# Kernel optimization log

Measured on AMD Instinct MI355X. Metric: run time of the kernel, lower is better.

The kernel has to match this reference:

```python
import jax, jax.numpy as jnp
import numpy as np

N = 50000; E = 800000
HID = 64; HEADS = 8; DH = HID // HEADS; L = 6
VOC = 512; NSIGN = 3; SIGN_DIM = 8; EDGE_DIM = 16; EPS = 1e-5


def setup_inputs() -> dict:
    key = jax.random.key(0)
    ks = jax.random.split(key, 24)
    s = 0.05
    rn = lambda k, sh: jax.random.normal(k, sh, jnp.float32) * s
    return dict(
        x_nodes=jax.random.randint(ks[0], (N, 4), 0, VOC),
        edge_index=jax.random.randint(ks[1], (2, E), 0, N),
        edge_label=jax.random.randint(ks[2], (E,), 0, VOC),
        edge_sign=jax.random.randint(ks[3], (E,), 0, NSIGN),
        emb_strand=rn(ks[4], (VOC, HID)),
        emb_pos=rn(ks[5], (4, HID)),
        emb_sign=rn(ks[6], (NSIGN, SIGN_DIM)),
        We=rn(ks[7], (HID + SIGN_DIM, EDGE_DIM)), be=jnp.zeros((EDGE_DIM,), jnp.float32),
        Wq=rn(ks[8], (L, HID, HID)), bq=jnp.zeros((L, HID), jnp.float32),
        Wk=rn(ks[9], (L, HID, HID)), bk=jnp.zeros((L, HID), jnp.float32),
        Wv=rn(ks[10], (L, HID, HID)), bv=jnp.zeros((L, HID), jnp.float32),
        Wedge=rn(ks[11], (L, EDGE_DIM, HID)),
        Wskip=rn(ks[12], (L, HID, HID)), bskip=jnp.zeros((L, HID), jnp.float32),
        ln_g=jnp.ones((L - 1, HID), jnp.float32), ln_b=jnp.zeros((L - 1, HID), jnp.float32),
        Wp=rn(ks[13], (HID, 2)), bp=jnp.zeros((2,), jnp.float32),
        Wv1=rn(ks[14], (HID, HID)), bv1=jnp.zeros((HID,), jnp.float32),
        Wv2=rn(ks[15], (HID, 1)), bv2=jnp.zeros((1,), jnp.float32),
    )


def _layernorm(x, g, b):
    mu = x.mean(-1, keepdims=True)
    var = jnp.mean((x - mu) ** 2, -1, keepdims=True)
    return g * (x - mu) / jnp.sqrt(var + EPS) + b


def reference(x_nodes, edge_index, edge_label, edge_sign,
              emb_strand, emb_pos, emb_sign, We, be,
              Wq, bq, Wk, bk, Wv, bv, Wedge, Wskip, bskip,
              ln_g, ln_b, Wp, bp, Wv1, bv1, Wv2, bv2):
    src, dst = edge_index[0], edge_index[1]
    # node features: per-crossing strand embeddings + positional embeddings, summed over 4 slots
    x = (emb_strand[x_nodes] + emb_pos[None, :, :]).sum(axis=1)  # [N, HID]
    # edge features: [strand_emb | sign_emb] -> Linear(24 -> 16)
    ef = jnp.concatenate([emb_strand[edge_label], emb_sign[edge_sign]], -1) @ We + be  # [E, 16]
    scale = 1.0 / jnp.sqrt(jnp.float32(DH))
    for l in range(L):
        q = (x @ Wq[l] + bq[l]).reshape(N, HEADS, DH)
        k = (x @ Wk[l] + bk[l]).reshape(N, HEADS, DH)
        v = (x @ Wv[l] + bv[l]).reshape(N, HEADS, DH)
        e = (ef @ Wedge[l]).reshape(E, HEADS, DH)  # lin_edge has no bias in PyG
        kj = k[src] + e  # [E, H, DH]
        alpha = (q[dst] * kj).sum(-1) * scale  # [E, H]
        m = jax.ops.segment_max(alpha, dst, num_segments=N)  # per-target softmax
        a = jnp.exp(alpha - m[dst])
        ssum = jax.ops.segment_sum(a, dst, num_segments=N)
        a = a / (ssum[dst] + 1e-16)
        msg = (v[src] + e) * a[:, :, None]
        out = jax.ops.segment_sum(msg, dst, num_segments=N).reshape(N, HID)
        out = out + x @ Wskip[l] + bskip[l]  # root_weight skip connection
        if l < L - 1:
            x = jax.nn.relu(_layernorm(out, ln_g[l], ln_b[l]))
        else:
            x = out
    policy = (x @ Wp + bp).reshape(1, -1)  # single-graph path: [1, 2N]
    g = x.mean(0, keepdims=True)  # [1, HID]
    val = jnp.tanh(jax.nn.relu(g @ Wv1 + bv1) @ Wv2 + bv2)  # [1, 1]
    return (policy, val)
```

## Files before the change

### kernel.cpp

```cpp
#include <hip/hip_runtime.h>
#include <math.h>

typedef _Float16 f16;
typedef _Float16 f16x8 __attribute__((ext_vector_type(8)));
typedef float f32x4 __attribute__((ext_vector_type(4)));

#define N_NODES 50000
#define N_EDGES 800000
#define HID 64
#define HEADS 8
#define DH 8
#define LAYERS 6
#define EDGE_DIM 16
#define SIGN_DIM 8
#define NSIGN 3
#define VOC 512
#define NCOMB (VOC * NSIGN)
#define EPS 1e-5f

#define NBUCK 196
#define BUCK_CAP 5120
#define BIN_EPB 4096
#define BIN_EPT 16
#define BIN_NBLK ((N_EDGES + BIN_EPB - 1) / BIN_EPB)

__device__ __forceinline__ float dot8(f16x8 a, f16x8 b, float c) {
#if __has_builtin(__builtin_amdgcn_fdot2)
    c = __builtin_amdgcn_fdot2(__builtin_shufflevector(a, a, 0, 1),
                               __builtin_shufflevector(b, b, 0, 1), c, false);
    c = __builtin_amdgcn_fdot2(__builtin_shufflevector(a, a, 2, 3),
                               __builtin_shufflevector(b, b, 2, 3), c, false);
    c = __builtin_amdgcn_fdot2(__builtin_shufflevector(a, a, 4, 5),
                               __builtin_shufflevector(b, b, 4, 5), c, false);
    c = __builtin_amdgcn_fdot2(__builtin_shufflevector(a, a, 6, 7),
                               __builtin_shufflevector(b, b, 6, 7), c, false);
#else
#pragma unroll
    for (int i = 0; i < 8; ++i) c += (float)a[i] * (float)b[i];
#endif
    return c;
}

__global__ __launch_bounds__(256) void k_node_feat(
    const int* __restrict__ xn, const float* __restrict__ emb_s,
    const float* __restrict__ emb_p, f16* __restrict__ x16) {
    int idx = blockIdx.x * 256 + threadIdx.x;
    if (idx >= N_NODES * HID) return;
    int n = idx >> 6, d = idx & 63;
    float acc = 0.f;
#pragma unroll
    for (int s = 0; s < 4; ++s) {
        int id = xn[n * 4 + s];
        acc += emb_s[id * HID + d] + emb_p[s * HID + d];
    }
    x16[idx] = (f16)acc;
}

__global__ __launch_bounds__(256) void k_tabTE(
    const float* __restrict__ emb_s, const float* __restrict__ emb_sg,
    const float* __restrict__ We, const float* __restrict__ be,
    const float* __restrict__ Wedge, f16* __restrict__ TE) {
    __shared__ float T[16][16];
    int t = threadIdx.x;
    int comb0 = blockIdx.x * 16;
    int cl = t >> 4, c = t & 15;
    int comb = comb0 + cl;
    int lb = comb / NSIGN, sg = comb % NSIGN;
    float acc = be[c];
    const float* er = emb_s + lb * HID;
#pragma unroll
    for (int j = 0; j < HID; ++j) acc += er[j] * We[j * EDGE_DIM + c];
    const float* sr = emb_sg + sg * SIGN_DIM;
#pragma unroll
    for (int j = 0; j < SIGN_DIM; ++j) acc += sr[j] * We[(HID + j) * EDGE_DIM + c];
    T[cl][c] = acc;
    __syncthreads();
    for (int l = 0; l < LAYERS; ++l) {
        const float* w = Wedge + l * EDGE_DIM * HID;
#pragma unroll
        for (int rep = 0; rep < 4; ++rep) {
            int idx = rep * 256 + t;
            int cml = idx >> 6, d = idx & 63;
            float a = 0.f;
#pragma unroll
            for (int j = 0; j < EDGE_DIM; ++j) a += T[cml][j] * w[j * HID + d];
            TE[((size_t)l * NCOMB + comb0 + cml) * HID + d] = (f16)a;
        }
    }
}

__global__ __launch_bounds__(256) void k_wprep(
    const float* __restrict__ Wq, const float* __restrict__ bq,
    const float* __restrict__ Wk, const float* __restrict__ bk,
    const float* __restrict__ Wv, const float* __restrict__ bv,
    const float* __restrict__ Ws, const float* __restrict__ bs,
    f16* __restrict__ wcatT, float* __restrict__ bcat) {
    int idx = blockIdx.x * 256 + threadIdx.x;
    if (idx >= LAYERS * 256 * HID) return;
    int l = idx >> 14;
    int r = idx & 16383;
    int c = r >> 6, kk = r & 63;
    int m = c >> 6, cc = c & 63;
    const float* W = (m == 0) ? Wq : (m == 1) ? Wk : (m == 2) ? Wv : Ws;
    wcatT[idx] = (f16)W[l * 4096 + kk * 64 + cc];
    if (kk == 0) {
        const float* B = (m == 0) ? bq : (m == 1) ? bk : (m == 2) ? bv : bs;
        bcat[l * 256 + c] = B[l * 64 + cc];
    }
}

__global__ __launch_bounds__(256) void k_bin(
    const int* __restrict__ src, const int* __restrict__ dst,
    const int* __restrict__ label, const int* __restrict__ sign,
    int* __restrict__ bcur, int2* __restrict__ buf) {
    __shared__ int hist[NBUCK];
    __shared__ int base[NBUCK];
    int t = threadIdx.x;
    for (int i = t; i < NBUCK; i += 256) hist[i] = 0;
    __syncthreads();
    int e0 = blockIdx.x * BIN_EPB;
    int pk[BIN_EPT], dl[BIN_EPT], bl[BIN_EPT], loc[BIN_EPT];
#pragma unroll
    for (int i = 0; i < BIN_EPT; ++i) {
        int e = e0 + i * 256 + t;
        bool vld = e < N_EDGES;
        int d = vld ? dst[e] : 0;
        bl[i] = d >> 8;
        dl[i] = d & 255;
        pk[i] = vld ? ((src[e] << 11) | (label[e] * NSIGN + sign[e])) : 0;
        loc[i] = vld ? atomicAdd(&hist[bl[i]], 1) : -1;
    }
    __syncthreads();
    if (t < NBUCK) {
        int h = hist[t];
        int gb = h ? atomicAdd(&bcur[t], h) : 0;
        base[t] = t * BUCK_CAP + gb;
    }
    __syncthreads();
#pragma unroll
    for (int i = 0; i < BIN_EPT; ++i)
        if (loc[i] >= 0) buf[base[bl[i]] + loc[i]] = make_int2(pk[i], dl[i]);
}

__global__ __launch_bounds__(256) void k_bscan(
    const int* __restrict__ bcur, int* __restrict__ bbase,
    int* __restrict__ rowptr, float* __restrict__ gsum) {
    __shared__ int ws[4];
    int t = threadIdx.x;
    int lane = t & 63, w = t >> 6;
    int v = (t < NBUCK) ? bcur[t] : 0;
    int incl = v;
#pragma unroll
    for (int o = 1; o < 64; o <<= 1) {
        int u = __shfl_up(incl, o);
        if (lane >= o) incl += u;
    }
    if (lane == 63) ws[w] = incl;
    __syncthreads();
    int woff = 0;
    for (int j = 0; j < w; ++j) woff += ws[j];
    if (t < NBUCK) bbase[t] = woff + incl - v;
    if (t == 0) rowptr[N_NODES] = N_EDGES;
    if (t < 64) gsum[t] = 0.f;
}

__global__ __launch_bounds__(256) void k_place(
    const int* __restrict__ bcur, const int* __restrict__ bbase,
    const int2* __restrict__ buf, int* __restrict__ rowptr,
    int* __restrict__ scomb) {
    __shared__ int hist[256];
    __shared__ int curs[256];
    __shared__ int ws[4];
    int t = threadIdx.x, b = blockIdx.x;
    hist[t] = 0;
    __syncthreads();
    int cnt = bcur[b];
    const int2* bb = buf + (size_t)b * BUCK_CAP;
    for (int i = t; i < cnt; i += 256) atomicAdd(&hist[bb[i].y], 1);
    __syncthreads();
    int v = hist[t];
    int lane = t & 63, w = t >> 6;
    int incl = v;
#pragma unroll
    for (int o = 1; o < 64; o <<= 1) {
        int u = __shfl_up(incl, o);
        if (lane >= o) incl += u;
    }
    if (lane == 63) ws[w] = incl;
    __syncthreads();
    int woff = 0;
    for (int j = 0; j < w; ++j) woff += ws[j];
    int start = bbase[b] + woff + incl - v;
    int n = (b << 8) + t;
    if (n < N_NODES) rowptr[n] = start;
    curs[t] = start;
    __syncthreads();
    for (int i = t; i < cnt; i += 256) {
        int2 r = bb[i];
        int pos = atomicAdd(&curs[r.y], 1);
        scomb[pos] = r.x;
    }
}

__global__ __launch_bounds__(256) void k_proj(
    const f16* __restrict__ x16, const f16* __restrict__ wcatT_l,
    const float* __restrict__ bcat_l,
    f16* __restrict__ q, f16* __restrict__ kv, f16* __restrict__ sk) {
    int t = threadIdx.x;
    int w = t >> 6, l = t & 63;
    int n0 = blockIdx.x * 16;
    int rowA = n0 + (l & 15);
    int kb = l >> 4;
    const f16* xr = x16 + (rowA << 6) + (kb << 3);
    f16x8 a0 = *(const f16x8*)(xr);
    f16x8 a1 = *(const f16x8*)(xr + 32);
    int c0 = w << 6;
    int rbase = n0 + ((l >> 4) << 2);
#pragma unroll
    for (int tt = 0; tt < 4; ++tt) {
        int cl = c0 + tt * 16 + (l & 15);
        const f16* wr = wcatT_l + (cl << 6) + (kb << 3);
        f16x8 b0 = *(const f16x8*)(wr);
        f16x8 b1 = *(const f16x8*)(wr + 32);
        f32x4 z = {0.f, 0.f, 0.f, 0.f};
        z = __builtin_amdgcn_mfma_f32_16x16x32_f16(a0, b0, z, 0, 0, 0);
        z = __builtin_amdgcn_mfma_f32_16x16x32_f16(a1, b1, z, 0, 0, 0);
        float bb = bcat_l[cl];
        int cc = cl & 63;
#pragma unroll
        for (int r = 0; r < 4; ++r) {
            int n = rbase + r;
            f16 val = (f16)(z[r] + bb);
            if (w == 0) q[(n << 6) + cc] = val;
            else if (w == 1) kv[(size_t)n * 128 + cc] = val;
            else if (w == 2) kv[(size_t)n * 128 + 64 + cc] = val;
            else sk[(n << 6) + cc] = val;
        }
    }
}

__global__ __launch_bounds__(256) void k_agg(
    const f16* __restrict__ q, const f16* __restrict__ kv,
    const f16* __restrict__ sk, const f16* __restrict__ te,
    const int* __restrict__ scomb, const int* __restrict__ rowptr,
    const float* __restrict__ ln_g, const float* __restrict__ ln_b,
    f16* __restrict__ xout, int do_ln,
    const float* __restrict__ Wp, const float* __restrict__ bp,
    float* __restrict__ pol) {
    int t = threadIdx.x;
    int wid = t >> 6, lane = t & 63;
    int n = blockIdx.x * 4 + wid;
    if (n >= N_NODES) return;
    int e = lane >> 3;
    int h = lane & 7;
    f16x8 qf = *(const f16x8*)(q + (n << 6) + (h << 3));
    int rs = rowptr[n], re = rowptr[n + 1];
    const float scale = 0.35355339059327373f;
    float lsum = 0.f;
    float acc0 = 0.f, acc1 = 0.f, acc2 = 0.f, acc3 = 0.f;
    float acc4 = 0.f, acc5 = 0.f, acc6 = 0.f, acc7 = 0.f;
    for (int j0 = rs; j0 < re; j0 += 16) {
        int ja = j0 + e, jb = j0 + 8 + e;
        bool va = ja < re, vb = jb < re;
        int pa = scomb[va ? ja : rs];
        int pb = scomb[vb ? jb : rs];
        const f16* kpa = kv + ((size_t)(pa >> 11) << 7) + (h << 3);
        const f16* kpb = kv + ((size_t)(pb >> 11) << 7) + (h << 3);
        f16x8 ka = *(const f16x8*)(kpa);
        f16x8 vaf = *(const f16x8*)(kpa + 64);
        f16x8 ta = *(const f16x8*)(te + ((pa & 2047) << 6) + (h << 3));
        f16x8 kb2 = *(const f16x8*)(kpb);
        f16x8 vbf = *(const f16x8*)(kpb + 64);
        f16x8 tb = *(const f16x8*)(te + ((pb & 2047) << 6) + (h << 3));
        float ala = dot8(qf, ka + ta, 0.f) * scale;
        float alb = dot8(qf, kb2 + tb, 0.f) * scale;
        float wa = va ? __expf(ala) : 0.f;
        float wb = vb ? __expf(alb) : 0.f;
        lsum += wa + wb;
        f16x8 vta = vaf + ta;
        f16x8 vtb = vbf + tb;
        acc0 += wa * (float)vta[0] + wb * (float)vtb[0];
        acc1 += wa * (float)vta[1] + wb * (float)vtb[1];
        acc2 += wa * (float)vta[2] + wb * (float)vtb[2];
        acc3 += wa * (float)vta[3] + wb * (float)vtb[3];
        acc4 += wa * (float)vta[4] + wb * (float)vtb[4];
        acc5 += wa * (float)vta[5] + wb * (float)vtb[5];
        acc6 += wa * (float)vta[6] + wb * (float)vtb[6];
        acc7 += wa * (float)vta[7] + wb * (float)vtb[7];
    }
#pragma unroll
    for (int o = 8; o < 64; o <<= 1) {
        lsum += __shfl_xor(lsum, o);
        acc0 += __shfl_xor(acc0, o);
        acc1 += __shfl_xor(acc1, o);
        acc2 += __shfl_xor(acc2, o);
        acc3 += __shfl_xor(acc3, o);
        acc4 += __shfl_xor(acc4, o);
        acc5 += __shfl_xor(acc5, o);
        acc6 += __shfl_xor(acc6, o);
        acc7 += __shfl_xor(acc7, o);
    }
    float av = acc0;
    av = (e == 1) ? acc1 : av;
    av = (e == 2) ? acc2 : av;
    av = (e == 3) ? acc3 : av;
    av = (e == 4) ? acc4 : av;
    av = (e == 5) ? acc5 : av;
    av = (e == 6) ? acc6 : av;
    av = (e == 7) ? acc7 : av;
    int d = (h << 3) + e;
    float outv = av / (lsum + 1e-16f) + (float)sk[(n << 6) + d];
    if (do_ln) {
        float ssum = outv;
#pragma unroll
        for (int o = 1; o < 64; o <<= 1) ssum += __shfl_xor(ssum, o);
        float mu = ssum * (1.f / 64.f);
        float dv = outv - mu;
        float vs = dv * dv;
#pragma unroll
        for (int o = 1; o < 64; o <<= 1) vs += __shfl_xor(vs, o);
        float var = vs * (1.f / 64.f);
        float yv = ln_g[d] * dv / sqrtf(var + EPS) + ln_b[d];
        outv = fmaxf(yv, 0.f);
        xout[(n << 6) + d] = (f16)outv;
    } else {
        xout[(n << 6) + d] = (f16)outv;
        float p0 = outv * Wp[d * 2 + 0];
        float p1 = outv * Wp[d * 2 + 1];
#pragma unroll
        for (int o = 1; o < 64; o <<= 1) {
            p0 += __shfl_xor(p0, o);
            p1 += __shfl_xor(p1, o);
        }
        if (lane == 0) {
            pol[n * 2 + 0] = p0 + bp[0];
            pol[n * 2 + 1] = p1 + bp[1];
        }
    }
}

__global__ __launch_bounds__(256) void k_colsum(const f16* __restrict__ x16, float* __restrict__ gsum) {
    __shared__ float sh[256];
    int t = threadIdx.x;
    int col = t & 63;
    float acc = 0.f;
    for (int n = blockIdx.x * 4 + (t >> 6); n < N_NODES; n += gridDim.x * 4)
        acc += (float)x16[(n << 6) + col];
    sh[t] = acc;
    __syncthreads();
    if (t < 64) {
        float s = sh[t] + sh[t + 64] + sh[t + 128] + sh[t + 192];
        atomicAdd(&gsum[t], s);
    }
}

__global__ __launch_bounds__(64) void k_value(
    const float* __restrict__ gsum, const float* __restrict__ Wv1,
    const float* __restrict__ bv1, const float* __restrict__ Wv2,
    const float* __restrict__ bv2, float* __restrict__ out) {
    int lane = threadIdx.x;
    float h = bv1[lane];
    for (int i = 0; i < HID; ++i) h += (gsum[i] * (1.f / N_NODES)) * Wv1[i * HID + lane];
    h = fmaxf(h, 0.f);
    float p = h * Wv2[lane];
#pragma unroll
    for (int o = 1; o < 64; o <<= 1) p += __shfl_xor(p, o);
    if (lane == 0) out[0] = tanhf(p + bv2[0]);
}

extern "C" void kernel_launch(void* const* d_in, const int* in_sizes, int n_in,
                              void* d_out, int out_size, void* d_ws, size_t ws_size,
                              hipStream_t stream) {
    const int* x_nodes = (const int*)d_in[0];
    const int* edge_index = (const int*)d_in[1];
    const int* edge_label = (const int*)d_in[2];
    const int* edge_sign = (const int*)d_in[3];
    const float* emb_strand = (const float*)d_in[4];
    const float* emb_pos = (const float*)d_in[5];
    const float* emb_sign = (const float*)d_in[6];
    const float* We = (const float*)d_in[7];
    const float* be = (const float*)d_in[8];
    const float* Wq = (const float*)d_in[9];
    const float* bq = (const float*)d_in[10];
    const float* Wk = (const float*)d_in[11];
    const float* bk = (const float*)d_in[12];
    const float* Wv = (const float*)d_in[13];
    const float* bv = (const float*)d_in[14];
    const float* Wedge = (const float*)d_in[15];
    const float* Wskip = (const float*)d_in[16];
    const float* bskip = (const float*)d_in[17];
    const float* ln_g = (const float*)d_in[18];
    const float* ln_b = (const float*)d_in[19];
    const float* Wp = (const float*)d_in[20];
    const float* bp = (const float*)d_in[21];
    const float* Wv1 = (const float*)d_in[22];
    const float* bv1 = (const float*)d_in[23];
    const float* Wv2 = (const float*)d_in[24];
    const float* bv2 = (const float*)d_in[25];
    float* out = (float*)d_out;

    const int* src = edge_index;
    const int* dst = edge_index + N_EDGES;

    char* ws = (char*)d_ws;
    size_t off = 0;
    auto alloc = [&](size_t bytes) -> void* {
        void* p = ws + off;
        off += (bytes + 255) & ~(size_t)255;
        return p;
    };
    f16* x16 = (f16*)alloc((size_t)N_NODES * HID * 2);
    f16* q = (f16*)alloc((size_t)N_NODES * HID * 2);
    f16* kv = (f16*)alloc((size_t)N_NODES * 128 * 2);
    f16* sk = (f16*)alloc((size_t)N_NODES * HID * 2);
    int* scomb = (int*)alloc((size_t)N_EDGES * 4);
    int2* binbuf = (int2*)alloc((size_t)NBUCK * BUCK_CAP * 8);
    int* rowptr = (int*)alloc((size_t)(N_NODES + 1) * 4);
    int* bcur = (int*)alloc((size_t)NBUCK * 4);
    int* bbase = (int*)alloc((size_t)NBUCK * 4);
    f16* TE = (f16*)alloc((size_t)LAYERS * NCOMB * HID * 2);
    f16* wcatT = (f16*)alloc((size_t)LAYERS * 256 * HID * 2);
    float* bcat = (float*)alloc((size_t)LAYERS * 256 * 4);
    float* gsum = (float*)alloc(64 * 4);

    hipMemsetAsync(bcur, 0, (size_t)NBUCK * 4, stream);

    k_node_feat<<<(N_NODES * HID + 255) / 256, 256, 0, stream>>>(x_nodes, emb_strand, emb_pos, x16);
    k_tabTE<<<NCOMB / 16, 256, 0, stream>>>(emb_strand, emb_sign, We, be, Wedge, TE);
    k_wprep<<<(LAYERS * 256 * HID + 255) / 256, 256, 0, stream>>>(
        Wq, bq, Wk, bk, Wv, bv, Wskip, bskip, wcatT, bcat);
    k_bin<<<BIN_NBLK, 256, 0, stream>>>(src, dst, edge_label, edge_sign, bcur, binbuf);
    k_bscan<<<1, 256, 0, stream>>>(bcur, bbase, rowptr, gsum);
    k_place<<<NBUCK, 256, 0, stream>>>(bcur, bbase, binbuf, rowptr, scomb);

    for (int l = 0; l < LAYERS; ++l) {
        k_proj<<<N_NODES / 16, 256, 0, stream>>>(
            x16, wcatT + (size_t)l * 256 * HID, bcat + (size_t)l * 256, q, kv, sk);
        int do_ln = (l < LAYERS - 1) ? 1 : 0;
        const float* lg = do_ln ? (ln_g + (size_t)l * HID) : ln_g;
        const float* lb = do_ln ? (ln_b + (size_t)l * HID) : ln_b;
        k_agg<<<(N_NODES + 3) / 4, 256, 0, stream>>>(
            q, kv, sk, TE + (size_t)l * NCOMB * HID, scomb, rowptr,
            lg, lb, x16, do_ln, Wp, bp, out);
    }

    k_colsum<<<128, 256, 0, stream>>>(x16, gsum);
    k_value<<<1, 64, 0, stream>>>(gsum, Wv1, bv1, Wv2, bv2, out + 2 * N_NODES);
}
```

Measured before the change: 423.7 us.

## Fuse next-layer projection into aggregation kernel and merge setup kernels

The aggregation kernel for layers 0-4 now applies layernorm+relu, stages the 4 node rows in shared memory, and runs the next layer's QKV/skip projection with MFMA directly. This removes the separate projection launches and the x16 round trip through global memory. Q/KV/skip buffers are ping-ponged across layers. The three setup kernels and the memset are folded into one block-dispatched kernel. The fused projection pads each 4-row tile to 16 MFMA rows, wasting three quarters of the matrix work, and it adds a block-wide barrier after the irregular per-node aggregation.

```diff
diff --git a/kernel.cpp b/kernel.cpp
--- a/kernel.cpp
+++ b/kernel.cpp
@@ -24,6 +24,11 @@
 #define BIN_EPT 16
 #define BIN_NBLK ((N_EDGES + BIN_EPB - 1) / BIN_EPB)
 
+#define NF_BLK 12500
+#define WP_BLK 384
+#define TE_BLK (LAYERS * (NCOMB / 16))
+#define SETUP_BLK (NF_BLK + WP_BLK + TE_BLK + 1)
+
 __device__ __forceinline__ float dot8(f16x8 a, f16x8 b, float c) {
 #if __has_builtin(__builtin_amdgcn_fdot2)
     c = __builtin_amdgcn_fdot2(__builtin_shufflevector(a, a, 0, 1),
@@ -41,41 +46,63 @@
     return c;
 }
 
-__global__ __launch_bounds__(256) void k_node_feat(
+__global__ __launch_bounds__(256) void k_setup(
     const int* __restrict__ xn, const float* __restrict__ emb_s,
-    const float* __restrict__ emb_p, f16* __restrict__ x16) {
-    int idx = blockIdx.x * 256 + threadIdx.x;
-    if (idx >= N_NODES * HID) return;
-    int n = idx >> 6, d = idx & 63;
-    float acc = 0.f;
-#pragma unroll
-    for (int s = 0; s < 4; ++s) {
-        int id = xn[n * 4 + s];
-        acc += emb_s[id * HID + d] + emb_p[s * HID + d];
-    }
-    x16[idx] = (f16)acc;
-}
-
-__global__ __launch_bounds__(256) void k_tabTE(
-    const float* __restrict__ emb_s, const float* __restrict__ emb_sg,
-    const float* __restrict__ We, const float* __restrict__ be,
-    const float* __restrict__ Wedge, f16* __restrict__ TE) {
-    __shared__ float T[16][16];
-    int t = threadIdx.x;
-    int comb0 = blockIdx.x * 16;
-    int cl = t >> 4, c = t & 15;
-    int comb = comb0 + cl;
-    int lb = comb / NSIGN, sg = comb % NSIGN;
-    float acc = be[c];
-    const float* er = emb_s + lb * HID;
-#pragma unroll
-    for (int j = 0; j < HID; ++j) acc += er[j] * We[j * EDGE_DIM + c];
-    const float* sr = emb_sg + sg * SIGN_DIM;
-#pragma unroll
-    for (int j = 0; j < SIGN_DIM; ++j) acc += sr[j] * We[(HID + j) * EDGE_DIM + c];
-    T[cl][c] = acc;
-    __syncthreads();
-    for (int l = 0; l < LAYERS; ++l) {
+    const float* __restrict__ emb_p, f16* __restrict__ x16,
+    const float* __restrict__ Wq, const float* __restrict__ bq,
+    const float* __restrict__ Wk, const float* __restrict__ bk,
+    const float* __restrict__ Wv, const float* __restrict__ bv,
+    const float* __restrict__ Ws, const float* __restrict__ bs,
+    f16* __restrict__ wcatT, float* __restrict__ bcat,
+    const float* __restrict__ emb_sg, const float* __restrict__ We,
+    const float* __restrict__ be, const float* __restrict__ Wedge,
+    f16* __restrict__ TE, int* __restrict__ bcur) {
+    int b = blockIdx.x;
+    int t = threadIdx.x;
+    if (b < NF_BLK) {
+        int idx = b * 256 + t;
+        int n = idx >> 6, d = idx & 63;
+        float acc = 0.f;
+#pragma unroll
+        for (int s = 0; s < 4; ++s) {
+            int id = xn[n * 4 + s];
+            acc += emb_s[id * HID + d] + emb_p[s * HID + d];
+        }
+        x16[idx] = (f16)acc;
+        return;
+    }
+    b -= NF_BLK;
+    if (b < WP_BLK) {
+        int idx = b * 256 + t;
+        int l = idx >> 14;
+        int r = idx & 16383;
+        int c = r >> 6, kk = r & 63;
+        int m = c >> 6, cc = c & 63;
+        const float* W = (m == 0) ? Wq : (m == 1) ? Wk : (m == 2) ? Wv : Ws;
+        wcatT[idx] = (f16)W[l * 4096 + kk * 64 + cc];
+        if (kk == 0) {
+            const float* B = (m == 0) ? bq : (m == 1) ? bk : (m == 2) ? bv : bs;
+            bcat[l * 256 + c] = B[l * 64 + cc];
+        }
+        return;
+    }
+    b -= WP_BLK;
+    if (b < TE_BLK) {
+        __shared__ float T[16][16];
+        int l = b / (NCOMB / 16);
+        int comb0 = (b % (NCOMB / 16)) * 16;
+        int cl = t >> 4, c = t & 15;
+        int comb = comb0 + cl;
+        int lb = comb / NSIGN, sg = comb % NSIGN;
+        float acc = be[c];
+        const float* er = emb_s + lb * HID;
+#pragma unroll
+        for (int j = 0; j < HID; ++j) acc += er[j] * We[j * EDGE_DIM + c];
+        const float* sr = emb_sg + sg * SIGN_DIM;
+#pragma unroll
+        for (int j = 0; j < SIGN_DIM; ++j) acc += sr[j] * We[(HID + j) * EDGE_DIM + c];
+        T[cl][c] = acc;
+        __syncthreads();
         const float* w = Wedge + l * EDGE_DIM * HID;
 #pragma unroll
         for (int rep = 0; rep < 4; ++rep) {
@@ -86,27 +113,9 @@
             for (int j = 0; j < EDGE_DIM; ++j) a += T[cml][j] * w[j * HID + d];
             TE[((size_t)l * NCOMB + comb0 + cml) * HID + d] = (f16)a;
         }
-    }
-}
-
-__global__ __launch_bounds__(256) void k_wprep(
-    const float* __restrict__ Wq, const float* __restrict__ bq,
-    const float* __restrict__ Wk, const float* __restrict__ bk,
-    const float* __restrict__ Wv, const float* __restrict__ bv,
-    const float* __restrict__ Ws, const float* __restrict__ bs,
-    f16* __restrict__ wcatT, float* __restrict__ bcat) {
-    int idx = blockIdx.x * 256 + threadIdx.x;
-    if (idx >= LAYERS * 256 * HID) return;
-    int l = idx >> 14;
-    int r = idx & 16383;
-    int c = r >> 6, kk = r & 63;
-    int m = c >> 6, cc = c & 63;
-    const float* W = (m == 0) ? Wq : (m == 1) ? Wk : (m == 2) ? Wv : Ws;
-    wcatT[idx] = (f16)W[l * 4096 + kk * 64 + cc];
-    if (kk == 0) {
-        const float* B = (m == 0) ? bq : (m == 1) ? bk : (m == 2) ? bv : bs;
-        bcat[l * 256 + c] = B[l * 64 + cc];
-    }
+        return;
+    }
+    if (t < NBUCK) bcur[t] = 0;
 }
 
 __global__ __launch_bounds__(256) void k_bin(
@@ -239,20 +248,23 @@
     }
 }
 
-__global__ __launch_bounds__(256) void k_agg(
+__global__ __launch_bounds__(256) void k_aggP(
     const f16* __restrict__ q, const f16* __restrict__ kv,
     const f16* __restrict__ sk, const f16* __restrict__ te,
     const int* __restrict__ scomb, const int* __restrict__ rowptr,
     const float* __restrict__ ln_g, const float* __restrict__ ln_b,
-    f16* __restrict__ xout, int do_ln,
-    const float* __restrict__ Wp, const float* __restrict__ bp,
-    float* __restrict__ pol) {
+    const f16* __restrict__ wcat_nx, const float* __restrict__ bcat_nx,
+    f16* __restrict__ q_o, f16* __restrict__ kv_o, f16* __restrict__ sk_o) {
+    __shared__ __align__(16) f16 xs[16][64];
     int t = threadIdx.x;
     int wid = t >> 6, lane = t & 63;
-    int n = blockIdx.x * 4 + wid;
-    if (n >= N_NODES) return;
+    int n0 = blockIdx.x * 4;
+    int n = n0 + wid;
+    for (int i = t; i < 768; i += 256) ((f16*)xs)[256 + i] = (f16)0.f;
     int e = lane >> 3;
     int h = lane & 7;
+    int d = (h << 3) + e;
+    float skv = (float)sk[(n << 6) + d];
     f16x8 qf = *(const f16x8*)(q + (n << 6) + (h << 3));
     int rs = rowptr[n], re = rowptr[n + 1];
     const float scale = 0.35355339059327373f;
@@ -308,34 +320,131 @@
     av = (e == 5) ? acc5 : av;
     av = (e == 6) ? acc6 : av;
     av = (e == 7) ? acc7 : av;
+    float outv = av / (lsum + 1e-16f) + skv;
+    float ssum = outv;
+#pragma unroll
+    for (int o = 1; o < 64; o <<= 1) ssum += __shfl_xor(ssum, o);
+    float mu = ssum * (1.f / 64.f);
+    float dv = outv - mu;
+    float vs = dv * dv;
+#pragma unroll
+    for (int o = 1; o < 64; o <<= 1) vs += __shfl_xor(vs, o);
+    float var = vs * (1.f / 64.f);
+    float yv = ln_g[d] * dv / sqrtf(var + EPS) + ln_b[d];
+    xs[wid][d] = (f16)fmaxf(yv, 0.f);
+    __syncthreads();
+    int rowA = lane & 15;
+    int kb = lane >> 4;
+    f16x8 a0 = *(const f16x8*)(&xs[rowA][kb << 3]);
+    f16x8 a1 = *(const f16x8*)(&xs[rowA][32 + (kb << 3)]);
+    int c0 = wid << 6;
+    bool stor = (lane >> 4) == 0;
+#pragma unroll
+    for (int tt = 0; tt < 4; ++tt) {
+        int cl = c0 + tt * 16 + (lane & 15);
+        const f16* wr = wcat_nx + (cl << 6) + (kb << 3);
+        f16x8 b0 = *(const f16x8*)(wr);
+        f16x8 b1 = *(const f16x8*)(wr + 32);
+        f32x4 z = {0.f, 0.f, 0.f, 0.f};
+        z = __builtin_amdgcn_mfma_f32_16x16x32_f16(a0, b0, z, 0, 0, 0);
+        z = __builtin_amdgcn_mfma_f32_16x16x32_f16(a1, b1, z, 0, 0, 0);
+        if (stor) {
+            float bb = bcat_nx[cl];
+            int cc = cl & 63;
+            int m = cl >> 6;
+#pragma unroll
+            for (int r = 0; r < 4; ++r) {
+                int nn = n0 + r;
+                f16 val = (f16)(z[r] + bb);
+                if (m == 0) q_o[(nn << 6) + cc] = val;
+                else if (m == 1) kv_o[(size_t)nn * 128 + cc] = val;
+                else if (m == 2) kv_o[(size_t)nn * 128 + 64 + cc] = val;
+                else sk_o[(nn << 6) + cc] = val;
+            }
+        }
+    }
+}
+
+__global__ __launch_bounds__(256) void k_aggF(
+    const f16* __restrict__ q, const f16* __restrict__ kv,
+    const f16* __restrict__ sk, const f16* __restrict__ te,
+    const int* __restrict__ scomb, const int* __restrict__ rowptr,
+    const float* __restrict__ Wp, const float* __restrict__ bp,
+    float* __restrict__ pol, f16* __restrict__ xout) {
+    int t = threadIdx.x;
+    int wid = t >> 6, lane = t & 63;
+    int n = blockIdx.x * 4 + wid;
+    int e = lane >> 3;
+    int h = lane & 7;
     int d = (h << 3) + e;
-    float outv = av / (lsum + 1e-16f) + (float)sk[(n << 6) + d];
-    if (do_ln) {
-        float ssum = outv;
-#pragma unroll
-        for (int o = 1; o < 64; o <<= 1) ssum += __shfl_xor(ssum, o);
-        float mu = ssum * (1.f / 64.f);
-        float dv = outv - mu;
-        float vs = dv * dv;
-#pragma unroll
-        for (int o = 1; o < 64; o <<= 1) vs += __shfl_xor(vs, o);
-        float var = vs * (1.f / 64.f);
-        float yv = ln_g[d] * dv / sqrtf(var + EPS) + ln_b[d];
-        outv = fmaxf(yv, 0.f);
-        xout[(n << 6) + d] = (f16)outv;
-    } else {
-        xout[(n << 6) + d] = (f16)outv;
-        float p0 = outv * Wp[d * 2 + 0];
-        float p1 = outv * Wp[d * 2 + 1];
-#pragma unroll
-        for (int o = 1; o < 64; o <<= 1) {
-            p0 += __shfl_xor(p0, o);
-            p1 += __shfl_xor(p1, o);
-        }
-        if (lane == 0) {
-            pol[n * 2 + 0] = p0 + bp[0];
-            pol[n * 2 + 1] = p1 + bp[1];
-        }
+    float skv = (float)sk[(n << 6) + d];
+    f16x8 qf = *(const f16x8*)(q + (n << 6) + (h << 3));
+    int rs = rowptr[n], re = rowptr[n + 1];
+    const float scale = 0.35355339059327373f;
+    float lsum = 0.f;
+    float acc0 = 0.f, acc1 = 0.f, acc2 = 0.f, acc3 = 0.f;
+    float acc4 = 0.f, acc5 = 0.f, acc6 = 0.f, acc7 = 0.f;
+    for (int j0 = rs; j0 < re; j0 += 16) {
+        int ja = j0 + e, jb = j0 + 8 + e;
+        bool va = ja < re, vb = jb < re;
+        int pa = scomb[va ? ja : rs];
+        int pb = scomb[vb ? jb : rs];
+        const f16* kpa = kv + ((size_t)(pa >> 11) << 7) + (h << 3);
+        const f16* kpb = kv + ((size_t)(pb >> 11) << 7) + (h << 3);
+        f16x8 ka = *(const f16x8*)(kpa);
+        f16x8 vaf = *(const f16x8*)(kpa + 64);
+        f16x8 ta = *(const f16x8*)(te + ((pa & 2047) << 6) + (h << 3));
+        f16x8 kb2 = *(const f16x8*)(kpb);
+        f16x8 vbf = *(const f16x8*)(kpb + 64);
+        f16x8 tb = *(const f16x8*)(te + ((pb & 2047) << 6) + (h << 3));
+        float ala = dot8(qf, ka + ta, 0.f) * scale;
+        float alb = dot8(qf, kb2 + tb, 0.f) * scale;
+        float wa = va ? __expf(ala) : 0.f;
+        float wb = vb ? __expf(alb) : 0.f;
+        lsum += wa + wb;
+        f16x8 vta = vaf + ta;
+        f16x8 vtb = vbf + tb;
+        acc0 += wa * (float)vta[0] + wb * (float)vtb[0];
+        acc1 += wa * (float)vta[1] + wb * (float)vtb[1];
+        acc2 += wa * (float)vta[2] + wb * (float)vtb[2];
+        acc3 += wa * (float)vta[3] + wb * (float)vtb[3];
+        acc4 += wa * (float)vta[4] + wb * (float)vtb[4];
+        acc5 += wa * (float)vta[5] + wb * (float)vtb[5];
+        acc6 += wa * (float)vta[6] + wb * (float)vtb[6];
+        acc7 += wa * (float)vta[7] + wb * (float)vtb[7];
+    }
+#pragma unroll
+    for (int o = 8; o < 64; o <<= 1) {
+        lsum += __shfl_xor(lsum, o);
+        acc0 += __shfl_xor(acc0, o);
+        acc1 += __shfl_xor(acc1, o);
+        acc2 += __shfl_xor(acc2, o);
+        acc3 += __shfl_xor(acc3, o);
+        acc4 += __shfl_xor(acc4, o);
+        acc5 += __shfl_xor(acc5, o);
+        acc6 += __shfl_xor(acc6, o);
+        acc7 += __shfl_xor(acc7, o);
+    }
+    float av = acc0;
+    av = (e == 1) ? acc1 : av;
+    av = (e == 2) ? acc2 : av;
+    av = (e == 3) ? acc3 : av;
+    av = (e == 4) ? acc4 : av;
+    av = (e == 5) ? acc5 : av;
+    av = (e == 6) ? acc6 : av;
+    av = (e == 7) ? acc7 : av;
+    float outv = av / (lsum + 1e-16f) + skv;
+    xout[(n << 6) + d] = (f16)outv;
+    float p0 = outv * Wp[d * 2 + 0];
+    float p1 = outv * Wp[d * 2 + 1];
+#pragma unroll
+    for (int o = 1; o < 64; o <<= 1) {
+        p0 += __shfl_xor(p0, o);
+        p1 += __shfl_xor(p1, o);
+    }
+    if (lane == 0) {
+        pol[n * 2 + 0] = p0 + bp[0];
+        pol[n * 2 + 1] = p1 + bp[1];
     }
 }
 
@@ -410,9 +519,12 @@
         return p;
     };
     f16* x16 = (f16*)alloc((size_t)N_NODES * HID * 2);
-    f16* q = (f16*)alloc((size_t)N_NODES * HID * 2);
-    f16* kv = (f16*)alloc((size_t)N_NODES * 128 * 2);
-    f16* sk = (f16*)alloc((size_t)N_NODES * HID * 2);
+    f16* qA = (f16*)alloc((size_t)N_NODES * HID * 2);
+    f16* kvA = (f16*)alloc((size_t)N_NODES * 128 * 2);
+    f16* skA = (f16*)alloc((size_t)N_NODES * HID * 2);
+    f16* qB = (f16*)alloc((size_t)N_NODES * HID * 2);
+    f16* kvB = (f16*)alloc((size_t)N_NODES * 128 * 2);
+    f16* skB = (f16*)alloc((size_t)N_NODES * HID * 2);
     int* scomb = (int*)alloc((size_t)N_EDGES * 4);
     int2* binbuf = (int2*)alloc((size_t)NBUCK * BUCK_CAP * 8);
     int* rowptr = (int*)alloc((size_t)(N_NODES + 1) * 4);
@@ -423,26 +535,30 @@
     float* bcat = (float*)alloc((size_t)LAYERS * 256 * 4);
     float* gsum = (float*)alloc(64 * 4);
 
-    hipMemsetAsync(bcur, 0, (size_t)NBUCK * 4, stream);
-
-    k_node_feat<<<(N_NODES * HID + 255) / 256, 256, 0, stream>>>(x_nodes, emb_strand, emb_pos, x16);
-    k_tabTE<<<NCOMB / 16, 256, 0, stream>>>(emb_strand, emb_sign, We, be, Wedge, TE);
-    k_wprep<<<(LAYERS * 256 * HID + 255) / 256, 256, 0, stream>>>(
-        Wq, bq, Wk, bk, Wv, bv, Wskip, bskip, wcatT, bcat);
+    k_setup<<<SETUP_BLK, 256, 0, stream>>>(
+        x_nodes, emb_strand, emb_pos, x16,
+        Wq, bq, Wk, bk, Wv, bv, Wskip, bskip, wcatT, bcat,
+        emb_sign, We, be, Wedge, TE, bcur);
     k_bin<<<BIN_NBLK, 256, 0, stream>>>(src, dst, edge_label, edge_sign, bcur, binbuf);
     k_bscan<<<1, 256, 0, stream>>>(bcur, bbase, rowptr, gsum);
     k_place<<<NBUCK, 256, 0, stream>>>(bcur, bbase, binbuf, rowptr, scomb);
 
-    for (int l = 0; l < LAYERS; ++l) {
-        k_proj<<<N_NODES / 16, 256, 0, stream>>>(
-            x16, wcatT + (size_t)l * 256 * HID, bcat + (size_t)l * 256, q, kv, sk);
-        int do_ln = (l < LAYERS - 1) ? 1 : 0;
-        const float* lg = do_ln ? (ln_g + (size_t)l * HID) : ln_g;
-        const float* lb = do_ln ? (ln_b + (size_t)l * HID) : ln_b;
-        k_agg<<<(N_NODES + 3) / 4, 256, 0, stream>>>(
-            q, kv, sk, TE + (size_t)l * NCOMB * HID, scomb, rowptr,
-            lg, lb, x16, do_ln, Wp, bp, out);
-    }
+    k_proj<<<N_NODES / 16, 256, 0, stream>>>(x16, wcatT, bcat, qA, kvA, skA);
+
+    f16 *qi = qA, *kvi = kvA, *ski = skA, *qo = qB, *kvo = kvB, *sko = skB;
+    for (int l = 0; l < LAYERS - 1; ++l) {
+        k_aggP<<<N_NODES / 4, 256, 0, stream>>>(
+            qi, kvi, ski, TE + (size_t)l * NCOMB * HID, scomb, rowptr,
+            ln_g + (size_t)l * HID, ln_b + (size_t)l * HID,
+            wcatT + (size_t)(l + 1) * 256 * HID, bcat + (size_t)(l + 1) * 256,
+            qo, kvo, sko);
+        f16* tq = qi; qi = qo; qo = tq;
+        f16* tk = kvi; kvi = kvo; kvo = tk;
+        f16* ts = ski; ski = sko; sko = ts;
+    }
+    k_aggF<<<N_NODES / 4, 256, 0, stream>>>(
+        qi, kvi, ski, TE + (size_t)(LAYERS - 1) * NCOMB * HID, scomb, rowptr,
+        Wp, bp, out, x16);
 
     k_colsum<<<128, 256, 0, stream>>>(x16, gsum);
     k_value<<<1, 64, 0, stream>>>(gsum, Wv1, bv1, Wv2, bv2, out + 2 * N_NODES);
```

New measurement: 535.1 us. 1.26x slower.
